# Kernel tuning notes

Measured on AMD Instinct MI355X. Metric: run time of the kernel, lower is better.

Reference implementation:

```python
import jax, jax.numpy as jnp
import numpy as np

B, T, C = 4, 2048, 1024
N_HEAD = 16
HEAD_DIM = C // N_HEAD


def setup_inputs() -> dict:
    key = jax.random.key(0)
    k1, k2, k3, k4, k5 = jax.random.split(key, 5)
    s = 0.02
    return {
        "x": jax.random.normal(k1, (B, T, C), dtype=jnp.float32),
        "w_attn": jax.random.normal(k2, (C, 3 * C), dtype=jnp.float32) * s,
        "b_attn": jnp.zeros((3 * C,), dtype=jnp.float32),
        "w_proj": jax.random.normal(k3, (C, C), dtype=jnp.float32) * s,
        "b_proj": jnp.zeros((C,), dtype=jnp.float32),
    }


def reference(x, w_attn, b_attn, w_proj, b_proj):
    Bb, Tt, Cc = x.shape
    qkv = x @ w_attn + b_attn                      # [B,T,3C]
    q, k, v = jnp.split(qkv, 3, axis=-1)
    # [B,T,C] -> [B,H,T,D]
    def heads(t):
        return t.reshape(Bb, Tt, N_HEAD, HEAD_DIM).transpose(0, 2, 1, 3)
    q, k, v = heads(q), heads(k), heads(v)
    scale = 1.0 / (HEAD_DIM ** 0.5)
    att = jnp.einsum('bhqd,bhkd->bhqk', q, k) * scale
    causal = jnp.tril(jnp.ones((Tt, Tt), dtype=bool))
    att = jnp.where(causal, att, -jnp.inf)
    att = jax.nn.softmax(att, axis=-1)             # dropout p=0.0 -> identity
    y = jnp.einsum('bhqk,bhkd->bhqd', att, v)
    y = y.transpose(0, 2, 1, 3).reshape(Bb, Tt, Cc)
    return y @ w_proj + b_proj
```

## Files before the change

### kernel.cpp

```cpp
#include <hip/hip_runtime.h>
#include <hip/hip_bf16.h>

typedef unsigned short u16;
typedef __bf16 bf16_t;
typedef bf16_t bf16x8 __attribute__((ext_vector_type(8)));
typedef float f32x4 __attribute__((ext_vector_type(4)));
typedef u16 u16x4 __attribute__((ext_vector_type(4)));

#define MFMA16(a, b, c) __builtin_amdgcn_mfma_f32_16x16x32_bf16((a), (b), (c), 0, 0, 0)

__device__ __forceinline__ u16 f2b(float f) {
  bf16_t h = (bf16_t)f;
  return __builtin_bit_cast(u16, h);
}

__device__ __forceinline__ void gload_lds16(const void* src, void* dst) {
  __builtin_amdgcn_global_load_lds(
      (const __attribute__((address_space(1))) void*)src,
      (__attribute__((address_space(3))) void*)dst, 16, 0, 0);
}

__device__ __forceinline__ bf16x8 frag_read(const u16* tile, int row, int kchunk) {
  int off = row * 128 + ((kchunk ^ (row & 7)) << 4);
  return *reinterpret_cast<const bf16x8*>(reinterpret_cast<const char*>(tile) + off);
}

__device__ __forceinline__ void stage128(const u16* g, int rowStrideElts, u16* tile, int tid) {
  int lane = tid & 63, w = tid >> 6;
#pragma unroll
  for (int i = 0; i < 4; ++i) {
    int r = w * 32 + i * 8 + (lane >> 3);
    int cs = (lane & 7) ^ (r & 7);
    gload_lds16(g + (size_t)r * rowStrideElts + cs * 8, tile + r * 64 + (lane & 7) * 8);
  }
}

__global__ __launch_bounds__(256) void cvt_f32_bf16(const float* __restrict__ in,
                                                    u16* __restrict__ out, int n4) {
  int i = blockIdx.x * 256 + threadIdx.x;
  if (i < n4) {
    float4 f = reinterpret_cast<const float4*>(in)[i];
    ushort4 o;
    o.x = f2b(f.x); o.y = f2b(f.y); o.z = f2b(f.z); o.w = f2b(f.w);
    reinterpret_cast<ushort4*>(out)[i] = o;
  }
}

__global__ __launch_bounds__(256) void transpose_cvt(const float* __restrict__ in,
                                                     u16* __restrict__ out, int K, int N) {
  __shared__ float t[32][33];
  int n0 = blockIdx.x * 32, k0 = blockIdx.y * 32;
  int tx = threadIdx.x & 31, ty = threadIdx.x >> 5;
#pragma unroll
  for (int i = 0; i < 32; i += 8)
    t[ty + i][tx] = in[(size_t)(k0 + ty + i) * N + n0 + tx];
  __syncthreads();
#pragma unroll
  for (int i = 0; i < 32; i += 8)
    out[(size_t)(n0 + ty + i) * K + k0 + tx] = f2b(t[tx][ty + i]);
}

__global__ __launch_bounds__(256) void gemm_qkv(const u16* __restrict__ xb,
                                                const u16* __restrict__ waT,
                                                const float* __restrict__ bias,
                                                u16* __restrict__ q, u16* __restrict__ kk,
                                                u16* __restrict__ vt) {
  __shared__ u16 lA[128 * 64];
  __shared__ u16 lB[128 * 64];
  int tid = threadIdx.x, lane = tid & 63, w = tid >> 6;
  int wr = w >> 1, wc = w & 1;
  int bm = blockIdx.x, bn = blockIdx.y;
  f32x4 acc[4][4] = {};
  const u16* gA = xb + (size_t)bm * 128 * 1024;
  const u16* gB = waT + (size_t)bn * 128 * 1024;
  for (int k0 = 0; k0 < 1024; k0 += 64) {
    stage128(gA + k0, 1024, lA, tid);
    stage128(gB + k0, 1024, lB, tid);
    __syncthreads();
#pragma unroll
    for (int s = 0; s < 2; ++s) {
      bf16x8 af[4], bfr[4];
#pragma unroll
      for (int mi = 0; mi < 4; ++mi)
        af[mi] = frag_read(lA, wr * 64 + mi * 16 + (lane & 15), (lane >> 4) + s * 4);
#pragma unroll
      for (int ni = 0; ni < 4; ++ni)
        bfr[ni] = frag_read(lB, wc * 64 + ni * 16 + (lane & 15), (lane >> 4) + s * 4);
#pragma unroll
      for (int mi = 0; mi < 4; ++mi)
#pragma unroll
        for (int ni = 0; ni < 4; ++ni)
          acc[mi][ni] = MFMA16(af[mi], bfr[ni], acc[mi][ni]);
    }
    __syncthreads();
  }
  int m0 = bm * 128 + wr * 64;
  int n0 = bn * 128 + wc * 64;
#pragma unroll
  for (int ni = 0; ni < 4; ++ni) {
    int col = n0 + ni * 16 + (lane & 15);
    float bv = bias[col];
    int part = col >> 10;
    int cin = col & 1023;
    int h = cin >> 6, d = cin & 63;
#pragma unroll
    for (int mi = 0; mi < 4; ++mi) {
#pragma unroll
      for (int j = 0; j < 4; ++j) {
        int row = m0 + mi * 16 + (lane >> 4) * 4 + j;
        int b = row >> 11, t = row & 2047;
        u16 hv = f2b(acc[mi][ni][j] + bv);
        if (part == 0)
          q[(((size_t)(b * 16 + h) * 2048 + t) << 6) + d] = hv;
        else if (part == 1)
          kk[(((size_t)(b * 16 + h) * 2048 + t) << 6) + d] = hv;
        else
          vt[(((size_t)(b * 16 + h) << 6) + d) * 2048 + t] = hv;
      }
    }
  }
}

__global__ __launch_bounds__(256) void gemm_proj(const u16* __restrict__ att,
                                                 const u16* __restrict__ wpT,
                                                 const float* __restrict__ bias,
                                                 float* __restrict__ out) {
  __shared__ u16 lA[128 * 64];
  __shared__ u16 lB[128 * 64];
  int tid = threadIdx.x, lane = tid & 63, w = tid >> 6;
  int wr = w >> 1, wc = w & 1;
  int bm = blockIdx.x, bn = blockIdx.y;
  f32x4 acc[4][4] = {};
  const u16* gA = att + (size_t)bm * 128 * 1024;
  const u16* gB = wpT + (size_t)bn * 128 * 1024;
  for (int k0 = 0; k0 < 1024; k0 += 64) {
    stage128(gA + k0, 1024, lA, tid);
    stage128(gB + k0, 1024, lB, tid);
    __syncthreads();
#pragma unroll
    for (int s = 0; s < 2; ++s) {
      bf16x8 af[4], bfr[4];
#pragma unroll
      for (int mi = 0; mi < 4; ++mi)
        af[mi] = frag_read(lA, wr * 64 + mi * 16 + (lane & 15), (lane >> 4) + s * 4);
#pragma unroll
      for (int ni = 0; ni < 4; ++ni)
        bfr[ni] = frag_read(lB, wc * 64 + ni * 16 + (lane & 15), (lane >> 4) + s * 4);
#pragma unroll
      for (int mi = 0; mi < 4; ++mi)
#pragma unroll
        for (int ni = 0; ni < 4; ++ni)
          acc[mi][ni] = MFMA16(af[mi], bfr[ni], acc[mi][ni]);
    }
    __syncthreads();
  }
  int m0 = bm * 128 + wr * 64;
  int n0 = bn * 128 + wc * 64;
#pragma unroll
  for (int ni = 0; ni < 4; ++ni) {
    int col = n0 + ni * 16 + (lane & 15);
    float bv = bias[col];
#pragma unroll
    for (int mi = 0; mi < 4; ++mi)
#pragma unroll
      for (int j = 0; j < 4; ++j) {
        int row = m0 + mi * 16 + (lane >> 4) * 4 + j;
        out[(size_t)row * 1024 + col] = acc[mi][ni][j] + bv;
      }
  }
}


__device__ __forceinline__ void stage_kv(const u16* kb, const u16* vb, int kt,
                                         u16* lK, u16* lV, int tid) {
  int lane = tid & 63, w = tid >> 6;
#pragma unroll
  for (int i = 0; i < 2; ++i) {
    int r = w * 16 + i * 8 + (lane >> 3);
    int cs = (lane & 7) ^ (r & 7);
    gload_lds16(kb + (size_t)(kt * 64 + r) * 64 + cs * 8, lK + r * 64 + (lane & 7) * 8);
    gload_lds16(vb + (size_t)r * 2048 + kt * 64 + cs * 8, lV + r * 64 + (lane & 7) * 8);
  }
}

__global__ __launch_bounds__(256, 3) void attn_fwd(const u16* __restrict__ q,
                                                   const u16* __restrict__ kk,
                                                   const u16* __restrict__ vt,
                                                   u16* __restrict__ att) {
  __shared__ u16 lK[2][64 * 64];
  __shared__ u16 lV[2][64 * 64];
  __shared__ u16 lP[4][16 * 64];
  int tid = threadIdx.x, lane = tid & 63, w = tid >> 6;
  int ln = lane & 15, g = lane >> 4;
  int gh = g >> 1, gl = g & 1;
  int bh = blockIdx.x;
  int qtA = blockIdx.y;
  int qtB = 31 - qtA;
  const u16* qb = q + (size_t)bh * 2048 * 64;
  const u16* kb = kk + (size_t)bh * 2048 * 64;
  const u16* vb = vt + (size_t)bh * 64 * 2048;
  int q0A = qtA * 64 + w * 16;
  int q0B = qtB * 64 + w * 16;
  u16* lPw = &lP[w][0];
  int prow = ln * 128;
  int xorq = (ln & 7) << 4;

  bf16x8 aqA[2], aqB[2];
  {
    const u16* pa = qb + (size_t)(q0A + ln) * 64 + g * 8;
    const u16* pb = qb + (size_t)(q0B + ln) * 64 + g * 8;
    aqA[0] = *reinterpret_cast<const bf16x8*>(pa);
    aqA[1] = *reinterpret_cast<const bf16x8*>(pa + 32);
    aqB[0] = *reinterpret_cast<const bf16x8*>(pb);
    aqB[1] = *reinterpret_cast<const bf16x8*>(pb + 32);
  }

  float mA = -1e30f, lA = 0.f, mB = -1e30f, lB = 0.f;
  f32x4 oA[4] = {}, oB[4] = {};

  constexpr float SCL = 0.18033688011112042f;

  auto proc_state = [&](f32x4* sf, float& m_r, float& l_r, f32x4* o,
                        bool domask, int k0, int qg, const u16* Vt) {
#pragma unroll
    for (int kc = 0; kc < 4; ++kc) sf[kc] *= SCL;
    if (domask) {
#pragma unroll
      for (int kc = 0; kc < 4; ++kc)
#pragma unroll
        for (int j = 0; j < 4; ++j)
          if (k0 + kc * 16 + g * 4 + j > qg) sf[kc][j] = -1e30f;
    }
    f32x4 m4;
#pragma unroll
    for (int j = 0; j < 4; ++j)
      m4[j] = fmaxf(fmaxf(sf[0][j], sf[1][j]), fmaxf(sf[2][j], sf[3][j]));
    float mx = fmaxf(fmaxf(m4[0], m4[1]), fmaxf(m4[2], m4[3]));
    mx = fmaxf(mx, __shfl_xor(mx, 16, 64));
    mx = fmaxf(mx, __shfl_xor(mx, 32, 64));
    if (!__all(mx - m_r <= 8.f)) {
      float mn = fmaxf(m_r, mx);
      float sc = exp2f(m_r - mn);
      m_r = mn;
      l_r *= sc;
#pragma unroll
      for (int dc = 0; dc < 4; ++dc) o[dc] *= sc;
    }
    float rs = 0.f;
#pragma unroll
    for (int kc = 0; kc < 4; ++kc) {
      u16x4 v4;
#pragma unroll
      for (int j = 0; j < 4; ++j) {
        float p = exp2f(sf[kc][j] - m_r);
        rs += p;
        v4[j] = f2b(p);
      }
      *reinterpret_cast<u16x4*>(reinterpret_cast<char*>(lPw) + prow +
                                ((((kc << 1) + gh) << 4) ^ xorq) + gl * 8) = v4;
    }
    rs += __shfl_xor(rs, 16, 64);
    rs += __shfl_xor(rs, 32, 64);
    l_r += rs;
    asm volatile("s_waitcnt lgkmcnt(0)" ::: "memory");
    __builtin_amdgcn_sched_barrier(0);
    __builtin_amdgcn_wave_barrier();
    bf16x8 bp0 = frag_read(lPw, ln, g);
    bf16x8 bp1 = frag_read(lPw, ln, g + 4);
    __builtin_amdgcn_sched_barrier(0);
    __builtin_amdgcn_s_setprio(1);
#pragma unroll
    for (int dc = 0; dc < 4; ++dc) {
      o[dc] = MFMA16(frag_read(Vt, dc * 16 + ln, g), bp0, o[dc]);
      o[dc] = MFMA16(frag_read(Vt, dc * 16 + ln, g + 4), bp1, o[dc]);
    }
    __builtin_amdgcn_s_setprio(0);
  };

  stage_kv(kb, vb, 0, &lK[0][0], &lV[0][0], tid);

  for (int kt = 0; kt <= qtB; ++kt) {
    int cur = kt & 1;
    __syncthreads();
    if (kt < qtB) stage_kv(kb, vb, kt + 1, &lK[cur ^ 1][0], &lV[cur ^ 1][0], tid);
    const u16* Kt = &lK[cur][0];
    const u16* Vt = &lV[cur][0];
    bool doA = (kt <= qtA);

    f32x4 sB[4], sA[4];
    __builtin_amdgcn_s_setprio(1);
#pragma unroll
    for (int kc = 0; kc < 4; ++kc) {
      f32x4 zB = {}, zA = {};
#pragma unroll
      for (int s = 0; s < 2; ++s) {
        bf16x8 kf = frag_read(Kt, kc * 16 + ln, g + 4 * s);
        zB = MFMA16(kf, aqB[s], zB);
        if (doA) zA = MFMA16(kf, aqA[s], zA);
      }
      sB[kc] = zB;
      sA[kc] = zA;
    }
    __builtin_amdgcn_s_setprio(0);

    proc_state(sB, mB, lB, oB, kt == qtB, kt * 64, q0B + ln, Vt);
    if (doA) proc_state(sA, mA, lA, oA, kt == qtA, kt * 64, q0A + ln, Vt);
  }

  int b = bh >> 4, h = bh & 15;
  auto epi = [&](const f32x4* o, float l_r, int q0w) {
    float inv = __builtin_amdgcn_rcpf(l_r);
#pragma unroll
    for (int dc = 0; dc < 4; ++dc) {
      u16x4 v4;
#pragma unroll
      for (int j = 0; j < 4; ++j) v4[j] = f2b(o[dc][j] * inv);
      *reinterpret_cast<u16x4*>(reinterpret_cast<char*>(lPw) + prow +
                                ((((dc << 1) + gh) << 4) ^ xorq) + gl * 8) = v4;
    }
    asm volatile("s_waitcnt lgkmcnt(0)" ::: "memory");
    __builtin_amdgcn_sched_barrier(0);
    __builtin_amdgcn_wave_barrier();
    bf16x8 r0 = frag_read(lPw, ln, g);
    bf16x8 r1 = frag_read(lPw, ln, g + 4);
    __builtin_amdgcn_sched_barrier(0);
    int t = q0w + ln;
    u16* dst = att + (size_t)(b * 2048 + t) * 1024 + h * 64;
    *reinterpret_cast<bf16x8*>(dst + g * 8) = r0;
    *reinterpret_cast<bf16x8*>(dst + 32 + g * 8) = r1;
  };
  epi(oB, lB, q0B);
  epi(oA, lA, q0A);
}

extern "C" void kernel_launch(void* const* d_in, const int* in_sizes, int n_in,
                              void* d_out, int out_size, void* d_ws, size_t ws_size,
                              hipStream_t stream) {
  const float* x = (const float*)d_in[0];
  const float* w_attn = (const float*)d_in[1];
  const float* b_attn = (const float*)d_in[2];
  const float* w_proj = (const float*)d_in[3];
  const float* b_proj = (const float*)d_in[4];
  float* out = (float*)d_out;

  u16* ws = (u16*)d_ws;
  u16* xb = ws;
  u16* waT = xb + 8388608;
  u16* wpT = waT + 3145728;
  u16* vtx = wpT + 1048576;
  u16* att = xb;
  u16* qx = (u16*)d_out;
  u16* kx = qx + 8388608;

  cvt_f32_bf16<<<8192, 256, 0, stream>>>(x, xb, 2097152);
  transpose_cvt<<<dim3(96, 32), 256, 0, stream>>>(w_attn, waT, 1024, 3072);
  transpose_cvt<<<dim3(32, 32), 256, 0, stream>>>(w_proj, wpT, 1024, 1024);
  gemm_qkv<<<dim3(64, 24), 256, 0, stream>>>(xb, waT, b_attn, qx, kx, vtx);
  attn_fwd<<<dim3(64, 16), 256, 0, stream>>>(qx, kx, vtx, att);
  gemm_proj<<<dim3(64, 8), 256, 0, stream>>>(att, wpT, b_proj, out);
}
```

Before: 221.8 us.

## Redistribute softmax probabilities via lane permutes instead of LDS round-trip

```diff
diff --git a/kernel.cpp b/kernel.cpp
--- a/kernel.cpp
+++ b/kernel.cpp
@@ -2,12 +2,18 @@
 #include <hip/hip_bf16.h>
 
 typedef unsigned short u16;
+typedef unsigned int u32;
 typedef __bf16 bf16_t;
 typedef bf16_t bf16x8 __attribute__((ext_vector_type(8)));
 typedef float f32x4 __attribute__((ext_vector_type(4)));
 typedef u16 u16x4 __attribute__((ext_vector_type(4)));
+typedef u32 u32x2 __attribute__((ext_vector_type(2)));
+typedef u32 u32x4 __attribute__((ext_vector_type(4)));
+typedef int intx2 __attribute__((ext_vector_type(2)));
 
 #define MFMA16(a, b, c) __builtin_amdgcn_mfma_f32_16x16x32_bf16((a), (b), (c), 0, 0, 0)
+
+#define QSCL 0.18033688011112042f
 
 __device__ __forceinline__ u16 f2b(float f) {
   bf16_t h = (bf16_t)f;
@@ -103,13 +109,14 @@
     int part = col >> 10;
     int cin = col & 1023;
     int h = cin >> 6, d = cin & 63;
+    float fct = (part == 0) ? QSCL : 1.0f;
 #pragma unroll
     for (int mi = 0; mi < 4; ++mi) {
 #pragma unroll
       for (int j = 0; j < 4; ++j) {
         int row = m0 + mi * 16 + (lane >> 4) * 4 + j;
         int b = row >> 11, t = row & 2047;
-        u16 hv = f2b(acc[mi][ni][j] + bv);
+        u16 hv = f2b((acc[mi][ni][j] + bv) * fct);
         if (part == 0)
           q[(((size_t)(b * 16 + h) * 2048 + t) << 6) + d] = hv;
         else if (part == 1)
@@ -183,16 +190,31 @@
   }
 }
 
-__global__ __launch_bounds__(256, 3) void attn_fwd(const u16* __restrict__ q,
+__device__ __forceinline__ bf16x8 pdist(u32 a0, u32 a1, u32 b0, u32 b1, bool odd) {
+  intx2 r0 = __builtin_amdgcn_permlane32_swap((int)a0, (int)b0, false, false);
+  intx2 r1 = __builtin_amdgcn_permlane32_swap((int)a1, (int)b1, false, false);
+  u32 x0 = __shfl_xor((u32)r0[1], 16, 64);
+  u32 x1 = __shfl_xor((u32)r1[1], 16, 64);
+  u32 y0 = __shfl_xor((u32)r0[0], 16, 64);
+  u32 y1 = __shfl_xor((u32)r1[0], 16, 64);
+  u32x4 f;
+  f[0] = odd ? x0 : (u32)r0[0];
+  f[1] = odd ? x1 : (u32)r1[0];
+  f[2] = odd ? (u32)r0[1] : y0;
+  f[3] = odd ? (u32)r1[1] : y1;
+  return __builtin_bit_cast(bf16x8, f);
+}
+
+__global__ __launch_bounds__(256, 4) void attn_fwd(const u16* __restrict__ q,
                                                    const u16* __restrict__ kk,
                                                    const u16* __restrict__ vt,
                                                    u16* __restrict__ att) {
   __shared__ u16 lK[2][64 * 64];
   __shared__ u16 lV[2][64 * 64];
-  __shared__ u16 lP[4][16 * 64];
   int tid = threadIdx.x, lane = tid & 63, w = tid >> 6;
   int ln = lane & 15, g = lane >> 4;
   int gh = g >> 1, gl = g & 1;
+  bool godd = (g & 1) != 0;
   int bh = blockIdx.x;
   int qtA = blockIdx.y;
   int qtB = 31 - qtA;
@@ -201,9 +223,6 @@
   const u16* vb = vt + (size_t)bh * 64 * 2048;
   int q0A = qtA * 64 + w * 16;
   int q0B = qtB * 64 + w * 16;
-  u16* lPw = &lP[w][0];
-  int prow = ln * 128;
-  int xorq = (ln & 7) << 4;
 
   bf16x8 aqA[2], aqB[2];
   {
@@ -218,12 +237,9 @@
   float mA = -1e30f, lA = 0.f, mB = -1e30f, lB = 0.f;
   f32x4 oA[4] = {}, oB[4] = {};
 
-  constexpr float SCL = 0.18033688011112042f;
-
-  auto proc_state = [&](f32x4* sf, float& m_r, float& l_r, f32x4* o,
-                        bool domask, int k0, int qg, const u16* Vt) {
-#pragma unroll
-    for (int kc = 0; kc < 4; ++kc) sf[kc] *= SCL;
+  auto softmax_state = [&](f32x4* sf, float& m_r, float& l_r, f32x4* o,
+                           bool domask, int k0, int qg,
+                           bf16x8& pf0, bf16x8& pf1) {
     if (domask) {
 #pragma unroll
       for (int kc = 0; kc < 4; ++kc)
@@ -235,46 +251,35 @@
 #pragma unroll
     for (int j = 0; j < 4; ++j)
       m4[j] = fmaxf(fmaxf(sf[0][j], sf[1][j]), fmaxf(sf[2][j], sf[3][j]));
-    float mx = fmaxf(fmaxf(m4[0], m4[1]), fmaxf(m4[2], m4[3]));
-    mx = fmaxf(mx, __shfl_xor(mx, 16, 64));
-    mx = fmaxf(mx, __shfl_xor(mx, 32, 64));
-    if (!__all(mx - m_r <= 8.f)) {
-      float mn = fmaxf(m_r, mx);
-      float sc = exp2f(m_r - mn);
-      m_r = mn;
+    float mxl = fmaxf(fmaxf(m4[0], m4[1]), fmaxf(m4[2], m4[3]));
+    if (!__all(mxl - m_r <= 8.f)) {
+      float mx = fmaxf(mxl, __shfl_xor(mxl, 16, 64));
+      mx = fmaxf(mx, __shfl_xor(mx, 32, 64));
+      mx = fmaxf(m_r, mx);
+      float sc = __builtin_amdgcn_exp2f(m_r - mx);
+      m_r = mx;
       l_r *= sc;
 #pragma unroll
       for (int dc = 0; dc < 4; ++dc) o[dc] *= sc;
     }
+    u32 d0[4], d1[4];
     float rs = 0.f;
 #pragma unroll
     for (int kc = 0; kc < 4; ++kc) {
       u16x4 v4;
 #pragma unroll
       for (int j = 0; j < 4; ++j) {
-        float p = exp2f(sf[kc][j] - m_r);
+        float p = __builtin_amdgcn_exp2f(sf[kc][j] - m_r);
         rs += p;
         v4[j] = f2b(p);
       }
-      *reinterpret_cast<u16x4*>(reinterpret_cast<char*>(lPw) + prow +
-                                ((((kc << 1) + gh) << 4) ^ xorq) + gl * 8) = v4;
-    }
-    rs += __shfl_xor(rs, 16, 64);
-    rs += __shfl_xor(rs, 32, 64);
+      u32x2 dd = __builtin_bit_cast(u32x2, v4);
+      d0[kc] = dd[0];
+      d1[kc] = dd[1];
+    }
     l_r += rs;
-    asm volatile("s_waitcnt lgkmcnt(0)" ::: "memory");
-    __builtin_amdgcn_sched_barrier(0);
-    __builtin_amdgcn_wave_barrier();
-    bf16x8 bp0 = frag_read(lPw, ln, g);
-    bf16x8 bp1 = frag_read(lPw, ln, g + 4);
-    __builtin_amdgcn_sched_barrier(0);
-    __builtin_amdgcn_s_setprio(1);
-#pragma unroll
-    for (int dc = 0; dc < 4; ++dc) {
-      o[dc] = MFMA16(frag_read(Vt, dc * 16 + ln, g), bp0, o[dc]);
-      o[dc] = MFMA16(frag_read(Vt, dc * 16 + ln, g + 4), bp1, o[dc]);
-    }
-    __builtin_amdgcn_s_setprio(0);
+    pf0 = pdist(d0[0], d1[0], d0[1], d1[1], godd);
+    pf1 = pdist(d0[2], d1[2], d0[3], d1[3], godd);
   };
 
   stage_kv(kb, vb, 0, &lK[0][0], &lV[0][0], tid);
@@ -303,13 +308,34 @@
     }
     __builtin_amdgcn_s_setprio(0);
 
-    proc_state(sB, mB, lB, oB, kt == qtB, kt * 64, q0B + ln, Vt);
-    if (doA) proc_state(sA, mA, lA, oA, kt == qtA, kt * 64, q0A + ln, Vt);
-  }
-
+    bf16x8 pB0, pB1, pA0, pA1;
+    softmax_state(sB, mB, lB, oB, kt == qtB, kt * 64, q0B + ln, pB0, pB1);
+    if (doA) softmax_state(sA, mA, lA, oA, kt == qtA, kt * 64, q0A + ln, pA0, pA1);
+
+    __builtin_amdgcn_s_setprio(1);
+#pragma unroll
+    for (int dc = 0; dc < 4; ++dc) {
+      bf16x8 v0 = frag_read(Vt, dc * 16 + ln, g);
+      bf16x8 v1 = frag_read(Vt, dc * 16 + ln, g + 4);
+      oB[dc] = MFMA16(v0, pB0, oB[dc]);
+      oB[dc] = MFMA16(v1, pB1, oB[dc]);
+      if (doA) {
+        oA[dc] = MFMA16(v0, pA0, oA[dc]);
+        oA[dc] = MFMA16(v1, pA1, oA[dc]);
+      }
+    }
+    __builtin_amdgcn_s_setprio(0);
+  }
+
+  __syncthreads();
+  u16* lPw = &lK[0][0] + w * 1024;
+  int prow = ln * 128;
+  int xorq = (ln & 7) << 4;
   int b = bh >> 4, h = bh & 15;
   auto epi = [&](const f32x4* o, float l_r, int q0w) {
-    float inv = __builtin_amdgcn_rcpf(l_r);
+    float lt = l_r + __shfl_xor(l_r, 16, 64);
+    lt += __shfl_xor(lt, 32, 64);
+    float inv = __builtin_amdgcn_rcpf(lt);
 #pragma unroll
     for (int dc = 0; dc < 4; ++dc) {
       u16x4 v4;
```

Result: faster. 209.1 us (-5.7%).
